# Performance work log

Measured on AMD Instinct MI355X. Metric: run time of the kernel, lower is better.

Reference implementation:

```python
import jax, jax.numpy as jnp
import numpy as np

HID = 128

def _sage(h, src, dst, Wl, bl, Wr, n):
    # PyG SAGEConv (mean aggr): out = lin_l(mean_{j in N(i)} h_j) + lin_r(h_i)
    msg = h[src]                                   # [E, H] gather
    s = jax.ops.segment_sum(msg, dst, num_segments=n)
    cnt = jax.ops.segment_sum(jnp.ones_like(dst, dtype=h.dtype), dst, num_segments=n)
    m = s / jnp.maximum(cnt, 1.0)[:, None]
    return m @ Wl + bl + h @ Wr

def setup_inputs() -> dict:
    key = jax.random.key(0)
    ks = jax.random.split(key, 20)
    NP, NC, E = 20000, 80000, 1600000
    N = NP + NC
    inp = {
        'x_pol_dyn': jax.random.normal(ks[0], (NP, 64), jnp.float32),
        'pol_state_idx': jax.random.randint(ks[1], (NP,), 0, 50),
        'x_comp_dyn': jax.random.normal(ks[2], (NC, 96), jnp.float32),
        'comp_sector_idx': jax.random.randint(ks[3], (NC,), 0, 12),
        'comp_ind_idx': jax.random.randint(ks[4], (NC,), 0, 150),
        'edge_index': jax.random.randint(ks[5], (2, E), 0, N),
        'state_emb': jax.random.normal(ks[6], (50, 8), jnp.float32) * 0.1,
        'sector_emb': jax.random.normal(ks[7], (12, 8), jnp.float32) * 0.1,
        'ind_emb': jax.random.normal(ks[8], (150, 8), jnp.float32) * 0.1,
        'W_pol': jax.random.normal(ks[9], (64 + 8, HID), jnp.float32) * 0.05,
        'b_pol': jnp.zeros((HID,), jnp.float32),
        'W_comp': jax.random.normal(ks[10], (96 + 16, HID), jnp.float32) * 0.05,
        'b_comp': jnp.zeros((HID,), jnp.float32),
        'Wl1': jax.random.normal(ks[11], (HID, HID), jnp.float32) * 0.05,
        'bl1': jnp.zeros((HID,), jnp.float32),
        'Wr1': jax.random.normal(ks[12], (HID, HID), jnp.float32) * 0.05,
        'Wl2': jax.random.normal(ks[13], (HID, HID), jnp.float32) * 0.05,
        'bl2': jnp.zeros((HID,), jnp.float32),
        'Wr2': jax.random.normal(ks[14], (HID, HID), jnp.float32) * 0.05,
    }
    return inp

def reference(x_pol_dyn, pol_state_idx, x_comp_dyn, comp_sector_idx, comp_ind_idx,
              edge_index, state_emb, sector_emb, ind_emb,
              W_pol, b_pol, W_comp, b_comp, Wl1, bl1, Wr1, Wl2, bl2, Wr2):
    pol_feat = jnp.concatenate([x_pol_dyn, state_emb[pol_state_idx]], axis=-1)
    comp_feat = jnp.concatenate([x_comp_dyn, sector_emb[comp_sector_idx], ind_emb[comp_ind_idx]], axis=-1)
    h_pol = jax.nn.relu(pol_feat @ W_pol + b_pol)
    h_comp = jax.nn.relu(comp_feat @ W_comp + b_comp)
    # dropout is identity in eval mode
    h = jnp.concatenate([h_pol, h_comp], axis=0)
    n = h.shape[0]
    src, dst = edge_index[0], edge_index[1]
    h = jax.nn.relu(_sage(h, src, dst, Wl1, bl1, Wr1, n))
    h = _sage(h, src, dst, Wl2, bl2, Wr2, n)
    np_ = h_pol.shape[0]
    return h[:np_], h[np_:]
```

## Files before the change

kernel.cpp:

```cpp
#include <hip/hip_runtime.h>

#define NP 20000
#define NC 80000
#define NN 100000
#define NE 1600000
#define HD 128
#define MAXDEG 64
#define BKT 391
#define BINB 391

typedef unsigned short ushort_t;
typedef unsigned int uint_t;

typedef __attribute__((ext_vector_type(8))) short bf16x8;
typedef __attribute__((ext_vector_type(4))) float f32x4;

__device__ __forceinline__ ushort_t f2bf(float f) {
  uint_t u = __builtin_bit_cast(uint_t, f);
  u = (u + 0x7FFF + ((u >> 16) & 1)) >> 16;
  return (ushort_t)u;
}
__device__ __forceinline__ float bf_lo(uint_t p) {
  return __builtin_bit_cast(float, p << 16);
}
__device__ __forceinline__ float bf_hi(uint_t p) {
  return __builtin_bit_cast(float, p & 0xFFFF0000u);
}
__device__ __forceinline__ uint4 pack8(float4 lo, float4 hi) {
  ushort_t t[8];
  t[0] = f2bf(lo.x); t[1] = f2bf(lo.y); t[2] = f2bf(lo.z); t[3] = f2bf(lo.w);
  t[4] = f2bf(hi.x); t[5] = f2bf(hi.y); t[6] = f2bf(hi.z); t[7] = f2bf(hi.w);
  return *(uint4*)t;
}

__device__ __forceinline__ void pack_tile(const float* __restrict__ W,
                                          ushort_t* __restrict__ P, int KF,
                                          int KB, int task) {
  int t = task / (KB * 64);
  int rem = task - t * KB * 64;
  int kb = rem >> 6;
  int lane = rem & 63;
  int k0 = kb * 32 + ((lane >> 4) << 3);
  int c = t * 16 + (lane & 15);
  ushort_t tmp[8];
#pragma unroll
  for (int j = 0; j < 8; ++j) {
    int k = k0 + j;
    tmp[j] = (k < KF) ? f2bf(W[(size_t)k * HD + c]) : (ushort_t)0;
  }
  *(uint4*)(P + (size_t)task * 8) = *(uint4*)tmp;
}

#define PACKB 46
__global__ __launch_bounds__(256) void prep_k(
    const int* __restrict__ dst, int* __restrict__ hist2t,
    const float* __restrict__ Wl1, const float* __restrict__ Wr1,
    const float* __restrict__ Wl2, const float* __restrict__ Wr2,
    const float* __restrict__ W_comp, const float* __restrict__ W_pol,
    ushort_t* __restrict__ wl1p, ushort_t* __restrict__ wr1p,
    ushort_t* __restrict__ wl2p, ushort_t* __restrict__ wr2p,
    ushort_t* __restrict__ wcompp, ushort_t* __restrict__ wpolp) {
  __shared__ int hist[BKT];
  int blk = blockIdx.x;
  int tid = threadIdx.x;
  if (blk < BINB) {
    for (int t = tid; t < BKT; t += 256) hist[t] = 0;
    __syncthreads();
    int base = blk * 4096;
#pragma unroll
    for (int q = 0; q < 16; ++q) {
      int e = base + q * 256 + tid;
      if (e < NE) atomicAdd(&hist[dst[e] >> 8], 1);
    }
    __syncthreads();
    for (int t = tid; t < BKT; t += 256)
      hist2t[(size_t)t * BINB + blk] = hist[t];
    return;
  }
  int pb = blk - BINB;
  if (pb < 8) pack_tile(Wl1, wl1p, 128, 4, pb * 256 + tid);
  else if (pb < 16) pack_tile(Wr1, wr1p, 128, 4, (pb - 8) * 256 + tid);
  else if (pb < 24) pack_tile(Wl2, wl2p, 128, 4, (pb - 16) * 256 + tid);
  else if (pb < 32) pack_tile(Wr2, wr2p, 128, 4, (pb - 24) * 256 + tid);
  else if (pb < 40) pack_tile(W_comp, wcompp, 112, 4, (pb - 32) * 256 + tid);
  else pack_tile(W_pol, wpolp, 72, 3, (pb - 40) * 256 + tid);
}

__global__ __launch_bounds__(64) void scanA_k(int* __restrict__ hist2t,
                                              int* __restrict__ bcnt) {
  int t = blockIdx.x;
  int lane = threadIdx.x;
  int* base = hist2t + (size_t)t * BINB;
  int carry = 0;
  for (int c = 0; c < 7; ++c) {
    int i = c * 64 + lane;
    int orig = (i < BINB) ? base[i] : 0;
    int v = orig;
#pragma unroll
    for (int off = 1; off < 64; off <<= 1) {
      int u = __shfl_up(v, off);
      if (lane >= off) v += u;
    }
    if (i < BINB) base[i] = v - orig + carry;
    carry += __shfl(v, 63);
  }
  if (lane == 0) bcnt[t] = carry;
}

__global__ __launch_bounds__(512) void scan_k(const int* __restrict__ bcnt,
                                              int* __restrict__ bstart) {
  __shared__ int s[512];
  int t = threadIdx.x;
  int v = (t < BKT) ? bcnt[t] : 0;
  s[t] = v;
  __syncthreads();
  for (int off = 1; off < 512; off <<= 1) {
    int x = (t >= off) ? s[t - off] : 0;
    __syncthreads();
    s[t] += x;
    __syncthreads();
  }
  if (t < BKT) bstart[t] = s[t] - v;
}

#define COMP_E (NC / 128)
#define POL_E ((NP + 127) / 128)
__global__ __launch_bounds__(512) void bin_enc_k(
    const int* __restrict__ src, const int* __restrict__ dst,
    const int* __restrict__ bstart, const int* __restrict__ hist2t,
    uint_t* __restrict__ ebuf,
    const float* __restrict__ x_comp, const int* __restrict__ sec,
    const int* __restrict__ ind, const float* __restrict__ semb,
    const float* __restrict__ iemb, const ushort_t* __restrict__ wcompp,
    const float* __restrict__ b_comp,
    const float* __restrict__ x_pol, const int* __restrict__ sidx,
    const float* __restrict__ stemb, const ushort_t* __restrict__ wpolp,
    const float* __restrict__ b_pol,
    ushort_t* __restrict__ h0) {
  __shared__ int hist[BKT];
  __shared__ int lscan[BKT];
  __shared__ int gbase[BKT];
  __shared__ int sv[512];
  __shared__ uint2 stage[4096];
  int blk = blockIdx.x;
  int tid = threadIdx.x;

  if (blk < BINB) {
    for (int t = tid; t < BKT; t += 512) hist[t] = 0;
    __syncthreads();
    int base = blk * 4096;
    int cntE = min(4096, NE - base);
    int ss[8], dd[8], rr[8];
#pragma unroll
    for (int q = 0; q < 8; ++q) {
      int e = base + q * 512 + tid;
      if (e < NE) {
        dd[q] = dst[e];
        ss[q] = src[e];
        rr[q] = atomicAdd(&hist[dd[q] >> 8], 1);
      } else {
        dd[q] = -1;
      }
    }
    __syncthreads();
    int hv = (tid < BKT) ? hist[tid] : 0;
    sv[tid] = hv;
    __syncthreads();
    for (int off = 1; off < 512; off <<= 1) {
      int x = (tid >= off) ? sv[tid - off] : 0;
      __syncthreads();
      sv[tid] += x;
      __syncthreads();
    }
    if (tid < BKT) {
      lscan[tid] = sv[tid] - hv;
      gbase[tid] = bstart[tid] + hist2t[(size_t)tid * BINB + blk];
    }
    __syncthreads();
#pragma unroll
    for (int q = 0; q < 8; ++q) {
      if (dd[q] >= 0) {
        int bb = dd[q] >> 8;
        stage[lscan[bb] + rr[q]] = make_uint2((uint_t)ss[q], (uint_t)dd[q]);
      }
    }
    __syncthreads();
    for (int j = tid; j < cntE; j += 512) {
      uint2 v = stage[j];
      int bb = v.y >> 8;
      ebuf[gbase[bb] + (j - lscan[bb])] = (v.x << 8) | (v.y & 255u);
    }
    return;
  }
  int lane = tid & 63;
  int wv = tid >> 6;
  int n16 = lane & 15, quad = lane >> 4;
  if (blk < BINB + COMP_E) {
    int rowbase = (blk - BINB) * 128 + wv * 16;
    int node = rowbase + n16;
    const float4* xr = (const float4*)(x_comp + (size_t)node * 96);
    uint4 a[4];
#pragma unroll
    for (int kb = 0; kb < 3; ++kb)
      a[kb] = pack8(xr[kb * 8 + quad * 2], xr[kb * 8 + quad * 2 + 1]);
    if (quad == 0) {
      const float4* er = (const float4*)(semb + (size_t)sec[node] * 8);
      a[3] = pack8(er[0], er[1]);
    } else if (quad == 1) {
      const float4* er = (const float4*)(iemb + (size_t)ind[node] * 8);
      a[3] = pack8(er[0], er[1]);
    } else {
      a[3] = make_uint4(0, 0, 0, 0);
    }
    const bf16x8* W = (const bf16x8*)wcompp;
    ushort_t* hb = h0 + (size_t)NP * HD;
#pragma unroll
    for (int t = 0; t < 8; ++t) {
      float bias = b_comp[t * 16 + n16];
      f32x4 acc = {bias, bias, bias, bias};
#pragma unroll
      for (int kb = 0; kb < 4; ++kb)
        acc = __builtin_amdgcn_mfma_f32_16x16x32_bf16(
            __builtin_bit_cast(bf16x8, a[kb]), W[(t * 4 + kb) * 64 + lane],
            acc, 0, 0, 0);
      int r0 = rowbase + quad * 4;
      int c = t * 16 + n16;
#pragma unroll
      for (int r = 0; r < 4; ++r)
        hb[(size_t)(r0 + r) * HD + c] = f2bf(fmaxf(acc[r], 0.f));
    }
    return;
  }
  {
    int rowbase = (blk - BINB - COMP_E) * 128 + wv * 16;
    if (rowbase >= NP) return;
    int node = rowbase + n16;
    const float4* xr = (const float4*)(x_pol + (size_t)node * 64);
    uint4 a[3];
#pragma unroll
    for (int kb = 0; kb < 2; ++kb)
      a[kb] = pack8(xr[kb * 8 + quad * 2], xr[kb * 8 + quad * 2 + 1]);
    if (quad == 0) {
      const float4* er = (const float4*)(stemb + (size_t)sidx[node] * 8);
      a[2] = pack8(er[0], er[1]);
    } else {
      a[2] = make_uint4(0, 0, 0, 0);
    }
    const bf16x8* W = (const bf16x8*)wpolp;
#pragma unroll
    for (int t = 0; t < 8; ++t) {
      float bias = b_pol[t * 16 + n16];
      f32x4 acc = {bias, bias, bias, bias};
#pragma unroll
      for (int kb = 0; kb < 3; ++kb)
        acc = __builtin_amdgcn_mfma_f32_16x16x32_bf16(
            __builtin_bit_cast(bf16x8, a[kb]), W[(t * 3 + kb) * 64 + lane],
            acc, 0, 0, 0);
      int r0 = rowbase + quad * 4;
      int c = t * 16 + n16;
#pragma unroll
      for (int r = 0; r < 4; ++r)
        h0[(size_t)(r0 + r) * HD + c] = f2bf(fmaxf(acc[r], 0.f));
    }
  }
}

__global__ __launch_bounds__(512) void build_k(const uint_t* __restrict__ ebuf,
                                               const int* __restrict__ bstart,
                                               const int* __restrict__ bcnt,
                                               int* __restrict__ col,
                                               int* __restrict__ cnt) {
  __shared__ int lcnt[256];
  int tid = threadIdx.x;
  int b = blockIdx.x;
  if (tid < 256) lcnt[tid] = 0;
  __syncthreads();
  int st = bstart[b];
  int cb = bcnt[b];
  for (int off = tid; off < cb; off += 512) {
    uint_t v = ebuf[st + off];
    int nl = v & 255u;
    int p = atomicAdd(&lcnt[nl], 1);
    if (p < MAXDEG) col[(size_t)((b << 8) | nl) * MAXDEG + p] = (int)(v >> 8);
  }
  __syncthreads();
  if (tid < 256) {
    int node = (b << 8) + tid;
    if (node < NN) cnt[node] = lcnt[tid];
  }
}

__global__ __launch_bounds__(256) void aggregate_k(
    const ushort_t* __restrict__ hbf, const int* __restrict__ cnt,
    const int* __restrict__ col, ushort_t* __restrict__ mbf) {
  const uint4* hrow = (const uint4*)hbf;
  int lane = threadIdx.x & 63;
  int iA = (blockIdx.x * 4 + (threadIdx.x >> 6)) * 2;
  int iB = iA + 1;
  int dA = min(cnt[iA], MAXDEG);
  int dB = min(cnt[iB], MAXDEG);
  int grp = lane >> 4;
  int l16 = lane & 15;
  float accA[8] = {0.f, 0.f, 0.f, 0.f, 0.f, 0.f, 0.f, 0.f};
  float accB[8] = {0.f, 0.f, 0.f, 0.f, 0.f, 0.f, 0.f, 0.f};
  int mycA = (lane < dA) ? col[(size_t)iA * MAXDEG + lane] : 0;
  int mycB = (lane < dB) ? col[(size_t)iB * MAXDEG + lane] : 0;
  int nch = (max(dA, dB) + 15) >> 4;
  for (int ch = 0; ch < nch; ++ch) {
    int j0 = ch * 16;
    uint4 pA[4], pB[4];
    bool vA[4], vB[4];
#pragma unroll
    for (int q = 0; q < 4; ++q) {
      int e = j0 + q * 4 + grp;
      vA[q] = e < dA;
      int s = __shfl(mycA, vA[q] ? e : 0);
      pA[q] = hrow[(size_t)s * 16 + l16];
    }
#pragma unroll
    for (int q = 0; q < 4; ++q) {
      int e = j0 + q * 4 + grp;
      vB[q] = e < dB;
      int s = __shfl(mycB, vB[q] ? e : 0);
      pB[q] = hrow[(size_t)s * 16 + l16];
    }
#pragma unroll
    for (int q = 0; q < 4; ++q) {
      if (vA[q]) {
        accA[0] += bf_lo(pA[q].x); accA[1] += bf_hi(pA[q].x);
        accA[2] += bf_lo(pA[q].y); accA[3] += bf_hi(pA[q].y);
        accA[4] += bf_lo(pA[q].z); accA[5] += bf_hi(pA[q].z);
        accA[6] += bf_lo(pA[q].w); accA[7] += bf_hi(pA[q].w);
      }
      if (vB[q]) {
        accB[0] += bf_lo(pB[q].x); accB[1] += bf_hi(pB[q].x);
        accB[2] += bf_lo(pB[q].y); accB[3] += bf_hi(pB[q].y);
        accB[4] += bf_lo(pB[q].z); accB[5] += bf_hi(pB[q].z);
        accB[6] += bf_lo(pB[q].w); accB[7] += bf_hi(pB[q].w);
      }
    }
  }
#pragma unroll
  for (int k = 0; k < 8; ++k) {
    accA[k] += __shfl_xor(accA[k], 16);
    accA[k] += __shfl_xor(accA[k], 32);
    accB[k] += __shfl_xor(accB[k], 16);
    accB[k] += __shfl_xor(accB[k], 32);
  }
  if (grp == 0) {
    float inv = 1.f / (float)max(dA, 1);
    ushort_t t[8];
#pragma unroll
    for (int k = 0; k < 8; ++k) t[k] = f2bf(accA[k] * inv);
    *(uint4*)(mbf + (size_t)iA * HD + l16 * 8) = *(uint4*)t;
  } else if (grp == 1) {
    float inv = 1.f / (float)max(dB, 1);
    ushort_t t[8];
#pragma unroll
    for (int k = 0; k < 8; ++k) t[k] = f2bf(accB[k] * inv);
    *(uint4*)(mbf + (size_t)iB * HD + l16 * 8) = *(uint4*)t;
  }
}

__global__ __launch_bounds__(256) void sage_mfma_k(
    const ushort_t* __restrict__ mb, const ushort_t* __restrict__ hb,
    const ushort_t* __restrict__ Wlp, const float* __restrict__ bl,
    const ushort_t* __restrict__ Wrp, float* __restrict__ outf,
    ushort_t* __restrict__ outb, int relu) {
  int lane = threadIdx.x & 63;
  int rowbase = blockIdx.x * 64 + (threadIdx.x >> 6) * 16;
  if (rowbase >= NN) return;
  int n16 = lane & 15, quad = lane >> 4;
  const uint4* mrow = (const uint4*)(mb + (size_t)(rowbase + n16) * HD);
  const uint4* hrow = (const uint4*)(hb + (size_t)(rowbase + n16) * HD);
  uint4 am[4], ah[4];
#pragma unroll
  for (int kb = 0; kb < 4; ++kb) {
    am[kb] = mrow[kb * 4 + quad];
    ah[kb] = hrow[kb * 4 + quad];
  }
  const bf16x8* WL = (const bf16x8*)Wlp;
  const bf16x8* WR = (const bf16x8*)Wrp;
#pragma unroll
  for (int t = 0; t < 8; ++t) {
    float bias = bl[t * 16 + n16];
    f32x4 acc = {bias, bias, bias, bias};
#pragma unroll
    for (int kb = 0; kb < 4; ++kb)
      acc = __builtin_amdgcn_mfma_f32_16x16x32_bf16(
          __builtin_bit_cast(bf16x8, am[kb]), WL[(t * 4 + kb) * 64 + lane],
          acc, 0, 0, 0);
#pragma unroll
    for (int kb = 0; kb < 4; ++kb)
      acc = __builtin_amdgcn_mfma_f32_16x16x32_bf16(
          __builtin_bit_cast(bf16x8, ah[kb]), WR[(t * 4 + kb) * 64 + lane],
          acc, 0, 0, 0);
    int r0 = rowbase + quad * 4;
    int c = t * 16 + n16;
#pragma unroll
    for (int r = 0; r < 4; ++r) {
      float v = acc[r];
      if (relu) v = fmaxf(v, 0.f);
      if (outb)
        outb[(size_t)(r0 + r) * HD + c] = f2bf(v);
      else
        outf[(size_t)(r0 + r) * HD + c] = v;
    }
  }
}

extern "C" void kernel_launch(void* const* d_in, const int* in_sizes, int n_in,
                              void* d_out, int out_size, void* d_ws,
                              size_t ws_size, hipStream_t stream) {
  const float* x_pol = (const float*)d_in[0];
  const int* pol_state_idx = (const int*)d_in[1];
  const float* x_comp = (const float*)d_in[2];
  const int* comp_sector = (const int*)d_in[3];
  const int* comp_ind = (const int*)d_in[4];
  const int* edge = (const int*)d_in[5];
  const float* state_emb = (const float*)d_in[6];
  const float* sector_emb = (const float*)d_in[7];
  const float* ind_emb = (const float*)d_in[8];
  const float* W_pol = (const float*)d_in[9];
  const float* b_pol = (const float*)d_in[10];
  const float* W_comp = (const float*)d_in[11];
  const float* b_comp = (const float*)d_in[12];
  const float* Wl1 = (const float*)d_in[13];
  const float* bl1 = (const float*)d_in[14];
  const float* Wr1 = (const float*)d_in[15];
  const float* Wl2 = (const float*)d_in[16];
  const float* bl2 = (const float*)d_in[17];
  const float* Wr2 = (const float*)d_in[18];

  const int* src = edge;
  const int* dst = edge + NE;

  const size_t HBYTES = (size_t)NN * HD * sizeof(ushort_t);
  char* ws = (char*)d_ws;
  ushort_t* m_bf = (ushort_t*)ws;
  ushort_t* h0_bf = (ushort_t*)(ws + HBYTES);
  ushort_t* h1_bf = (ushort_t*)(ws + 2 * HBYTES);
  int* col = (int*)(ws + 3 * HBYTES);
  uint_t* ebuf = (uint_t*)(col + (size_t)NN * MAXDEG);
  int* cnt = (int*)(ebuf + NE);
  ushort_t* wl1p = (ushort_t*)(cnt + NN);
  ushort_t* wr1p = wl1p + 16384;
  ushort_t* wl2p = wr1p + 16384;
  ushort_t* wr2p = wl2p + 16384;
  ushort_t* wcompp = wr2p + 16384;
  ushort_t* wpolp = wcompp + 16384;
  int* bcnt = (int*)(wpolp + 12288);
  int* bstart = bcnt + BKT;
  int* hist2t = bstart + BKT;

  float* out_f = (float*)d_out;

  prep_k<<<BINB + PACKB, 256, 0, stream>>>(dst, hist2t, Wl1, Wr1, Wl2, Wr2,
                                           W_comp, W_pol, wl1p, wr1p, wl2p,
                                           wr2p, wcompp, wpolp);
  scanA_k<<<BKT, 64, 0, stream>>>(hist2t, bcnt);
  scan_k<<<1, 512, 0, stream>>>(bcnt, bstart);
  bin_enc_k<<<BINB + COMP_E + POL_E, 512, 0, stream>>>(
      src, dst, bstart, hist2t, ebuf, x_comp, comp_sector, comp_ind,
      sector_emb, ind_emb, wcompp, b_comp, x_pol, pol_state_idx, state_emb,
      wpolp, b_pol, h0_bf);
  build_k<<<BKT, 512, 0, stream>>>(ebuf, bstart, bcnt, col, cnt);

  const int GB = (NN + 63) / 64;
  aggregate_k<<<NN / 8, 256, 0, stream>>>(h0_bf, cnt, col, m_bf);
  sage_mfma_k<<<GB, 256, 0, stream>>>(m_bf, h0_bf, wl1p, bl1, wr1p, nullptr,
                                      h1_bf, 1);

  aggregate_k<<<NN / 8, 256, 0, stream>>>(h1_bf, cnt, col, m_bf);
  sage_mfma_k<<<GB, 256, 0, stream>>>(m_bf, h1_bf, wl2p, bl2, wr2p, out_f,
                                      nullptr, 0);
}
```

Before: 333.8 us.

## Fuse neighbor mean aggregation with SAGE MFMA linear layers per 16-row tile

```diff
diff --git a/kernel.cpp b/kernel.cpp
--- a/kernel.cpp
+++ b/kernel.cpp
@@ -8,6 +8,7 @@
 #define MAXDEG 64
 #define BKT 391
 #define BINB 391
+
 
 typedef unsigned short ushort_t;
 typedef unsigned int uint_t;
@@ -290,12 +291,18 @@
   }
 }
 
-__global__ __launch_bounds__(256) void aggregate_k(
+__global__ __launch_bounds__(512) void agg_sage_k(
     const ushort_t* __restrict__ hbf, const int* __restrict__ cnt,
-    const int* __restrict__ col, ushort_t* __restrict__ mbf) {
+    const int* __restrict__ col, const ushort_t* __restrict__ Wlp,
+    const float* __restrict__ bl, const ushort_t* __restrict__ Wrp,
+    float* __restrict__ outf, ushort_t* __restrict__ outb, int relu) {
+  __shared__ __align__(16) ushort_t lm[16][136];
   const uint4* hrow = (const uint4*)hbf;
-  int lane = threadIdx.x & 63;
-  int iA = (blockIdx.x * 4 + (threadIdx.x >> 6)) * 2;
+  int tid = threadIdx.x;
+  int lane = tid & 63;
+  int wv = tid >> 6;
+  int rowbase = blockIdx.x * 16;
+  int iA = rowbase + wv * 2;
   int iB = iA + 1;
   int dA = min(cnt[iA], MAXDEG);
   int dB = min(cnt[iB], MAXDEG);
@@ -352,60 +359,49 @@
     ushort_t t[8];
 #pragma unroll
     for (int k = 0; k < 8; ++k) t[k] = f2bf(accA[k] * inv);
-    *(uint4*)(mbf + (size_t)iA * HD + l16 * 8) = *(uint4*)t;
+    *(uint4*)&lm[wv * 2][l16 * 8] = *(uint4*)t;
   } else if (grp == 1) {
     float inv = 1.f / (float)max(dB, 1);
     ushort_t t[8];
 #pragma unroll
     for (int k = 0; k < 8; ++k) t[k] = f2bf(accB[k] * inv);
-    *(uint4*)(mbf + (size_t)iB * HD + l16 * 8) = *(uint4*)t;
-  }
-}
-
-__global__ __launch_bounds__(256) void sage_mfma_k(
-    const ushort_t* __restrict__ mb, const ushort_t* __restrict__ hb,
-    const ushort_t* __restrict__ Wlp, const float* __restrict__ bl,
-    const ushort_t* __restrict__ Wrp, float* __restrict__ outf,
-    ushort_t* __restrict__ outb, int relu) {
-  int lane = threadIdx.x & 63;
-  int rowbase = blockIdx.x * 64 + (threadIdx.x >> 6) * 16;
-  if (rowbase >= NN) return;
-  int n16 = lane & 15, quad = lane >> 4;
-  const uint4* mrow = (const uint4*)(mb + (size_t)(rowbase + n16) * HD);
-  const uint4* hrow = (const uint4*)(hb + (size_t)(rowbase + n16) * HD);
+    *(uint4*)&lm[wv * 2 + 1][l16 * 8] = *(uint4*)t;
+  }
+  __syncthreads();
+
+  int t = wv;
+  int n16 = l16, quad = grp;
+  const uint4* hr = (const uint4*)(hbf + (size_t)(rowbase + n16) * HD);
   uint4 am[4], ah[4];
 #pragma unroll
   for (int kb = 0; kb < 4; ++kb) {
-    am[kb] = mrow[kb * 4 + quad];
-    ah[kb] = hrow[kb * 4 + quad];
+    am[kb] = *(const uint4*)&lm[n16][(kb * 4 + quad) * 8];
+    ah[kb] = hr[kb * 4 + quad];
   }
   const bf16x8* WL = (const bf16x8*)Wlp;
   const bf16x8* WR = (const bf16x8*)Wrp;
-#pragma unroll
-  for (int t = 0; t < 8; ++t) {
-    float bias = bl[t * 16 + n16];
-    f32x4 acc = {bias, bias, bias, bias};
-#pragma unroll
-    for (int kb = 0; kb < 4; ++kb)
-      acc = __builtin_amdgcn_mfma_f32_16x16x32_bf16(
-          __builtin_bit_cast(bf16x8, am[kb]), WL[(t * 4 + kb) * 64 + lane],
-          acc, 0, 0, 0);
-#pragma unroll
-    for (int kb = 0; kb < 4; ++kb)
-      acc = __builtin_amdgcn_mfma_f32_16x16x32_bf16(
-          __builtin_bit_cast(bf16x8, ah[kb]), WR[(t * 4 + kb) * 64 + lane],
-          acc, 0, 0, 0);
-    int r0 = rowbase + quad * 4;
-    int c = t * 16 + n16;
-#pragma unroll
-    for (int r = 0; r < 4; ++r) {
-      float v = acc[r];
-      if (relu) v = fmaxf(v, 0.f);
-      if (outb)
-        outb[(size_t)(r0 + r) * HD + c] = f2bf(v);
-      else
-        outf[(size_t)(r0 + r) * HD + c] = v;
-    }
+  float bias = bl[t * 16 + n16];
+  f32x4 acc = {bias, bias, bias, bias};
+#pragma unroll
+  for (int kb = 0; kb < 4; ++kb)
+    acc = __builtin_amdgcn_mfma_f32_16x16x32_bf16(
+        __builtin_bit_cast(bf16x8, am[kb]), WL[(t * 4 + kb) * 64 + lane],
+        acc, 0, 0, 0);
+#pragma unroll
+  for (int kb = 0; kb < 4; ++kb)
+    acc = __builtin_amdgcn_mfma_f32_16x16x32_bf16(
+        __builtin_bit_cast(bf16x8, ah[kb]), WR[(t * 4 + kb) * 64 + lane],
+        acc, 0, 0, 0);
+  int r0 = rowbase + quad * 4;
+  int c = t * 16 + n16;
+#pragma unroll
+  for (int r = 0; r < 4; ++r) {
+    float v = acc[r];
+    if (relu) v = fmaxf(v, 0.f);
+    if (outb)
+      outb[(size_t)(r0 + r) * HD + c] = f2bf(v);
+    else
+      outf[(size_t)(r0 + r) * HD + c] = v;
   }
 }
 
@@ -417,7 +413,6 @@
   const float* x_comp = (const float*)d_in[2];
   const int* comp_sector = (const int*)d_in[3];
   const int* comp_ind = (const int*)d_in[4];
-  const int* edge = (const int*)d_in[5];
   const float* state_emb = (const float*)d_in[6];
   const float* sector_emb = (const float*)d_in[7];
   const float* ind_emb = (const float*)d_in[8];
@@ -432,15 +427,14 @@
   const float* bl2 = (const float*)d_in[17];
   const float* Wr2 = (const float*)d_in[18];
 
-  const int* src = edge;
-  const int* dst = edge + NE;
+  const int* src = (const int*)d_in[5];
+  const int* dst = ((const int*)d_in[5]) + NE;
 
   const size_t HBYTES = (size_t)NN * HD * sizeof(ushort_t);
   char* ws = (char*)d_ws;
-  ushort_t* m_bf = (ushort_t*)ws;
-  ushort_t* h0_bf = (ushort_t*)(ws + HBYTES);
-  ushort_t* h1_bf = (ushort_t*)(ws + 2 * HBYTES);
-  int* col = (int*)(ws + 3 * HBYTES);
+  ushort_t* h0_bf = (ushort_t*)ws;
+  ushort_t* h1_bf = (ushort_t*)(ws + HBYTES);
+  int* col = (int*)(ws + 2 * HBYTES);
   uint_t* ebuf = (uint_t*)(col + (size_t)NN * MAXDEG);
   int* cnt = (int*)(ebuf + NE);
   ushort_t* wl1p = (ushort_t*)(cnt + NN);
@@ -466,12 +460,8 @@
       wpolp, b_pol, h0_bf);
   build_k<<<BKT, 512, 0, stream>>>(ebuf, bstart, bcnt, col, cnt);
 
-  const int GB = (NN + 63) / 64;
-  aggregate_k<<<NN / 8, 256, 0, stream>>>(h0_bf, cnt, col, m_bf);
-  sage_mfma_k<<<GB, 256, 0, stream>>>(m_bf, h0_bf, wl1p, bl1, wr1p, nullptr,
-                                      h1_bf, 1);
-
-  aggregate_k<<<NN / 8, 256, 0, stream>>>(h1_bf, cnt, col, m_bf);
-  sage_mfma_k<<<GB, 256, 0, stream>>>(m_bf, h1_bf, wl2p, bl2, wr2p, out_f,
-                                      nullptr, 0);
-}
+  agg_sage_k<<<NN / 16, 512, 0, stream>>>(h0_bf, cnt, col, wl1p, bl1, wr1p,
+                                          nullptr, h1_bf, 1);
+  agg_sage_k<<<NN / 16, 512, 0, stream>>>(h1_bf, cnt, col, wl2p, bl2, wr2p,
+                                          out_f, nullptr, 0);
+}
```

New measurement: 327.5 us. No clear change (-1.9%).
